# Performance work log

Hardware: AMD Instinct MI355X
Metric: run time of the kernel (lower is better)

## Reference

```python
import itertools
import jax, jax.numpy as jnp
import numpy as np

EPS = 1e-15
B, K, H, W = 64, 8, 128, 128


def setup_inputs() -> dict:
    key = jax.random.key(0)
    k1, k2 = jax.random.split(key)
    pred_masks = jax.random.uniform(k1, (B, K, H, W), dtype=jnp.float32)
    aug_masks = jax.random.uniform(k2, (B, K, H, W), dtype=jnp.float32)
    return {"pred_masks": pred_masks, "aug_masks": aug_masks}


def _mask_kl_div(pred, true):
    # true * (log(true+eps) - log(pred+eps)), mean over (H, W)
    return (true * (jnp.log(true + EPS) - jnp.log(pred + EPS))).mean(axis=(-2, -1))


# all K! permutations, precomputed once (K=8 -> 40320 perms)
_PERMS = jnp.asarray(np.array(list(itertools.permutations(range(K))), dtype=np.int32))


def reference(pred_masks, aug_masks):
    b, k, h, w = pred_masks.shape
    t = aug_masks  # targets are detached in torch for the cost matrix
    # Fused pairwise KL cost matrix (avoids the (B,K,K,H,W) broadcast):
    # C[b,i,j] = mean_hw[ t_j*log(t_j+eps) ] - mean_hw[ t_j*log(p_i+eps) ]
    ent = (t * jnp.log(t + EPS)).mean(axis=(-2, -1))          # (B, K) over j
    cross = jnp.einsum('bjhw,bihw->bij', t, jnp.log(pred_masks + EPS)) / (h * w)
    C = ent[:, None, :] - cross                                # (B, K, K)
    # exact linear assignment via exhaustive search over K! permutations
    rows = jnp.arange(k)
    costs = C[:, rows[None, :], _PERMS].sum(axis=-1)           # (B, K!)
    R2C = _PERMS[jnp.argmin(costs, axis=1)]                    # (B, K) col for each row
    # permute rows: out[b, i] = pred[b, argsort(R2C)[b, i]]
    row_perm = jnp.argsort(R2C, axis=1)
    pred_perm = jnp.take_along_axis(pred_masks, row_perm[:, :, None, None], axis=1)
    l = _mask_kl_div(pred_perm, t)                             # (B, K)
    return l.mean(), pred_perm[..., None]
```

## Files before the change

### kernel.cpp

```cpp
#include <hip/hip_runtime.h>


#define BB 64
#define KK 8
#define HW 16384
#define SPANS 16
#define SPAN 1024
#define NCH 4
#define CHUNK 256
#define EPSF 1e-15f

struct MaskTab {
    unsigned char masks[255];
    int off[9];
};

constexpr MaskTab make_tab() {
    MaskTab t{};
    int idx = 0;
    for (int p = 1; p <= 8; ++p) {
        t.off[p - 1] = idx;
        for (int m = 1; m < 256; ++m) {
            int c = 0;
            for (int b = 0; b < 8; ++b) c += (m >> b) & 1;
            if (c == p) t.masks[idx++] = (unsigned char)m;
        }
    }
    t.off[8] = idx;
    return t;
}

__constant__ MaskTab kTab = make_tab();

__device__ __forceinline__ float dot4(float4 t, float4 l) {
    return t.x * l.x + t.y * l.y + t.z * l.z + t.w * l.w;
}

__device__ __forceinline__ float4 log4(float4 a) {
    float4 r;
    r.x = __logf(a.x + EPSF); r.y = __logf(a.y + EPSF);
    r.z = __logf(a.z + EPSF); r.w = __logf(a.w + EPSF);
    return r;
}

__global__ __launch_bounds__(256) void cost_kernel(const float* __restrict__ pred,
                                                   const float* __restrict__ aug,
                                                   float* __restrict__ part,
                                                   float* __restrict__ out)
{
    __shared__ float tile[2][16][CHUNK];

    const int blk  = blockIdx.x;
    const int b    = blk >> 4;
    const int s    = blk & 15;
    const int tid  = threadIdx.x;
    const int wave = tid >> 6;
    const int lane = tid & 63;

    if (blk == 0 && tid == 0) out[0] = 0.f;

    const size_t base = (size_t)b * (KK * HW) + (size_t)s * SPAN;
    const int e4 = lane * 4;
    const int w2 = 2 * wave;

#define STAGE(c)                                                                          \
    {                                                                                     \
        const int pb_ = (c) & 1;                                                          \
        _Pragma("unroll")                                                                 \
        for (int m = 0; m < 4; ++m) {                                                     \
            const int vr = wave + 4 * m;                                                  \
            const float* g = ((vr < 8) ? (pred + base + (size_t)vr * HW)                  \
                                       : (aug + base + (size_t)(vr - 8) * HW))            \
                             + (c) * CHUNK + e4;                                          \
            __builtin_amdgcn_global_load_lds(                                             \
                (const __attribute__((address_space(1))) void*)g,                         \
                (__attribute__((address_space(3))) void*)&tile[pb_][vr][e4], 16, 0, 0);   \
        }                                                                                 \
    }

    STAGE(0)

    float acc[16];
#pragma unroll
    for (int v = 0; v < 16; ++v) acc[v] = 0.f;
    float e0 = 0.f, e1 = 0.f;

#pragma unroll
    for (int c = 0; c < NCH; ++c) {
        __syncthreads();
        if (c + 1 < NCH) STAGE(c + 1)

        const int pb = c & 1;
        const float4 la = log4(*(const float4*)&tile[pb][w2][e4]);
        const float4 lc = log4(*(const float4*)&tile[pb][w2 + 1][e4]);
#pragma unroll
        for (int j = 0; j < 8; ++j) {
            const float4 tv = *(const float4*)&tile[pb][8 + j][e4];
            acc[j]     += dot4(tv, la);
            acc[8 + j] += dot4(tv, lc);
            if (j == w2)     e0 += dot4(tv, log4(tv));
            if (j == w2 + 1) e1 += dot4(tv, log4(tv));
        }
    }
#undef STAGE

#pragma unroll
    for (int v = 0; v < 16; ++v) {
        float sv = acc[v];
#pragma unroll
        for (int d = 1; d < 64; d <<= 1) sv += __shfl_xor(sv, d);
        acc[v] = sv;
    }
#pragma unroll
    for (int d = 1; d < 64; d <<= 1) e0 += __shfl_xor(e0, d);
#pragma unroll
    for (int d = 1; d < 64; d <<= 1) e1 += __shfl_xor(e1, d);

    if (lane == 0) {
        float* dst = part + (size_t)blk * 72;
#pragma unroll
        for (int j = 0; j < 8; ++j) {
            dst[16 * wave + j]     = acc[j];
            dst[16 * wave + 8 + j] = acc[8 + j];
        }
        dst[64 + w2]     = e0;
        dst[64 + w2 + 1] = e1;
    }
}

__global__ __launch_bounds__(256) void permute_kernel(const float* __restrict__ pred,
                                                      const float* __restrict__ part,
                                                      float* __restrict__ out)
{
    __shared__ float red[72];
    __shared__ float C[64];
    __shared__ float dp[256];
    __shared__ int   choice[256];
    __shared__ int   inv8[8];

    const int p    = blockIdx.x;
    const int b    = p >> 3;
    const int tid  = threadIdx.x;

    const float* pb = part + (size_t)b * SPANS * 72;
    if (tid < 72) {
        float s = 0.f;
#pragma unroll
        for (int c = 0; c < SPANS; ++c) s += pb[c * 72 + tid];
        red[tid] = s;
    }
    if (tid == 0) dp[0] = 0.f;
    __syncthreads();
    if (tid < 64) C[tid] = red[64 + (tid & 7)] - red[tid];
    __syncthreads();

    const int grp = tid >> 3;
    const int j   = tid & 7;
    for (int lvl = 1; lvl <= 8; ++lvl) {
        const int start = kTab.off[lvl - 1];
        const int end   = kTab.off[lvl];
        const float* Crow = &C[(lvl - 1) * 8];
        for (int bse = start; bse < end; bse += 32) {
            const int mi = bse + grp;
            if (mi < end) {
                const int M = kTab.masks[mi];
                float v  = 1e30f;
                int   bj = 0;
                if (M & (1 << j)) {
                    v  = dp[M ^ (1 << j)] + Crow[j];
                    bj = j;
                }
#pragma unroll
                for (int d = 1; d < 8; d <<= 1) {
                    const float ov = __shfl_xor(v, d);
                    const int   oj = __shfl_xor(bj, d);
                    if (ov < v) { v = ov; bj = oj; }
                }
                if (j == 0) { dp[M] = v; choice[M] = bj; }
            }
        }
        __syncthreads();
    }

    if (tid == 0) {
        int mask = 255;
        for (int r = 7; r >= 0; --r) {
            const int jj = choice[mask];
            inv8[jj] = r;
            mask ^= 1 << jj;
        }
        if ((p & 7) == 0)
            atomicAdd(out, dp[255] * (1.0f / (16384.0f * 512.0f)));
    }
    __syncthreads();

    const int src_row = inv8[p & 7];
    const float* src  = pred + ((size_t)(b << 3) + src_row) * HW;
    float*      drow  = out + 1 + (size_t)p * HW;

#pragma unroll
    for (int m = 0; m < 16; ++m) {
        const int f = tid + 256 * m;
        const int e = 3 + 4 * f;
        if (f < 4095) {
            float4 v;
            v.x = src[e]; v.y = src[e + 1]; v.z = src[e + 2]; v.w = src[e + 3];
            *(float4*)(drow + e) = v;
        } else {
            drow[0] = src[0]; drow[1] = src[1]; drow[2] = src[2];
            drow[16383] = src[16383];
        }
    }
}

extern "C" void kernel_launch(void* const* d_in, const int* in_sizes, int n_in,
                              void* d_out, int out_size, void* d_ws, size_t ws_size,
                              hipStream_t stream) {
    const float* pred = (const float*)d_in[0];
    const float* aug  = (const float*)d_in[1];
    float* out = (float*)d_out;
    float* part = (float*)d_ws;

    cost_kernel<<<dim3(BB * SPANS), dim3(256), 0, stream>>>(pred, aug, part, out);
    permute_kernel<<<dim3(512), dim3(256), 0, stream>>>(pred, part, out);
}
```

Baseline: 122.4 us.

## Compute full 8x8 cost per thread with register accumulation and recursive-halving reduction

```diff
diff --git a/kernel.cpp b/kernel.cpp
--- a/kernel.cpp
+++ b/kernel.cpp
@@ -4,10 +4,8 @@
 #define BB 64
 #define KK 8
 #define HW 16384
-#define SPANS 16
-#define SPAN 1024
-#define NCH 4
-#define CHUNK 256
+#define SPANS 8
+#define SPAN 2048
 #define EPSF 1e-15f
 
 struct MaskTab {
@@ -48,83 +46,87 @@
                                                    float* __restrict__ part,
                                                    float* __restrict__ out)
 {
-    __shared__ float tile[2][16][CHUNK];
+    __shared__ float red[4][72];
 
     const int blk  = blockIdx.x;
-    const int b    = blk >> 4;
-    const int s    = blk & 15;
+    const int b    = blk >> 3;
+    const int s    = blk & 7;
     const int tid  = threadIdx.x;
     const int wave = tid >> 6;
     const int lane = tid & 63;
 
     if (blk == 0 && tid == 0) out[0] = 0.f;
 
-    const size_t base = (size_t)b * (KK * HW) + (size_t)s * SPAN;
-    const int e4 = lane * 4;
-    const int w2 = 2 * wave;
-
-#define STAGE(c)                                                                          \
-    {                                                                                     \
-        const int pb_ = (c) & 1;                                                          \
-        _Pragma("unroll")                                                                 \
-        for (int m = 0; m < 4; ++m) {                                                     \
-            const int vr = wave + 4 * m;                                                  \
-            const float* g = ((vr < 8) ? (pred + base + (size_t)vr * HW)                  \
-                                       : (aug + base + (size_t)(vr - 8) * HW))            \
-                             + (c) * CHUNK + e4;                                          \
-            __builtin_amdgcn_global_load_lds(                                             \
-                (const __attribute__((address_space(1))) void*)g,                         \
-                (__attribute__((address_space(3))) void*)&tile[pb_][vr][e4], 16, 0, 0);   \
-        }                                                                                 \
-    }
-
-    STAGE(0)
-
-    float acc[16];
-#pragma unroll
-    for (int v = 0; v < 16; ++v) acc[v] = 0.f;
-    float e0 = 0.f, e1 = 0.f;
-
-#pragma unroll
-    for (int c = 0; c < NCH; ++c) {
-        __syncthreads();
-        if (c + 1 < NCH) STAGE(c + 1)
-
-        const int pb = c & 1;
-        const float4 la = log4(*(const float4*)&tile[pb][w2][e4]);
-        const float4 lc = log4(*(const float4*)&tile[pb][w2 + 1][e4]);
+    const size_t base = (size_t)b * (KK * HW);
+
+    float acc[64];
+#pragma unroll
+    for (int v = 0; v < 64; ++v) acc[v] = 0.f;
+    float ent[8];
+#pragma unroll
+    for (int j = 0; j < 8; ++j) ent[j] = 0.f;
+
+#pragma unroll
+    for (int it = 0; it < 2; ++it) {
+        const int e = s * SPAN + (it * 256 + tid) * 4;
+        const float* pp = pred + base + e;
+        const float* ap = aug  + base + e;
+
+        float4 lp[8];
+#pragma unroll
+        for (int i = 0; i < 8; ++i)
+            lp[i] = log4(*(const float4*)(pp + (size_t)i * HW));
+
 #pragma unroll
         for (int j = 0; j < 8; ++j) {
-            const float4 tv = *(const float4*)&tile[pb][8 + j][e4];
-            acc[j]     += dot4(tv, la);
-            acc[8 + j] += dot4(tv, lc);
-            if (j == w2)     e0 += dot4(tv, log4(tv));
-            if (j == w2 + 1) e1 += dot4(tv, log4(tv));
-        }
-    }
-#undef STAGE
-
-#pragma unroll
-    for (int v = 0; v < 16; ++v) {
-        float sv = acc[v];
-#pragma unroll
-        for (int d = 1; d < 64; d <<= 1) sv += __shfl_xor(sv, d);
-        acc[v] = sv;
-    }
-#pragma unroll
-    for (int d = 1; d < 64; d <<= 1) e0 += __shfl_xor(e0, d);
-#pragma unroll
-    for (int d = 1; d < 64; d <<= 1) e1 += __shfl_xor(e1, d);
-
-    if (lane == 0) {
-        float* dst = part + (size_t)blk * 72;
-#pragma unroll
-        for (int j = 0; j < 8; ++j) {
-            dst[16 * wave + j]     = acc[j];
-            dst[16 * wave + 8 + j] = acc[8 + j];
-        }
-        dst[64 + w2]     = e0;
-        dst[64 + w2 + 1] = e1;
+            const float4 a  = *(const float4*)(ap + (size_t)j * HW);
+            ent[j] += dot4(a, log4(a));
+#pragma unroll
+            for (int i = 0; i < 8; ++i)
+                acc[i * 8 + j] += dot4(a, lp[i]);
+        }
+    }
+
+#pragma unroll
+    for (int r = 0; r < 6; ++r) {
+        const int d    = 1 << r;
+        const int half = 32 >> r;
+        const bool hi  = (lane & d) != 0;
+#pragma unroll
+        for (int k = 0; k < half; ++k) {
+            const float send = hi ? acc[k] : acc[k + half];
+            const float recv = __shfl_xor(send, d);
+            acc[k] = (hi ? acc[k + half] : acc[k]) + recv;
+        }
+    }
+
+#pragma unroll
+    for (int r = 0; r < 3; ++r) {
+        const int d    = 1 << r;
+        const int half = 4 >> r;
+        const bool hi  = (lane & d) != 0;
+#pragma unroll
+        for (int k = 0; k < half; ++k) {
+            const float send = hi ? ent[k] : ent[k + half];
+            const float recv = __shfl_xor(send, d);
+            ent[k] = (hi ? ent[k + half] : ent[k]) + recv;
+        }
+    }
+    float ev = ent[0];
+    ev += __shfl_xor(ev, 8);
+    ev += __shfl_xor(ev, 16);
+    ev += __shfl_xor(ev, 32);
+
+    const int vidx = ((lane & 1) << 5) | ((lane & 2) << 3) | ((lane & 4) << 1) |
+                     ((lane & 8) >> 1) | ((lane & 16) >> 3) | ((lane & 32) >> 5);
+    red[wave][vidx] = acc[0];
+    if (lane < 8)
+        red[wave][64 + (((lane & 1) << 2) | (lane & 2) | ((lane & 4) >> 2))] = ev;
+    __syncthreads();
+
+    if (tid < 72) {
+        const float ssum = red[0][tid] + red[1][tid] + red[2][tid] + red[3][tid];
+        part[(size_t)blk * 72 + tid] = ssum;
     }
 }
 
```

After: 118.9 us. 1.03x faster.
